# Performance work log

Measured on AMD Instinct MI355X. Metric: run time of the kernel, lower is better.

The kernel has to match this reference:

```python
import jax, jax.numpy as jnp
import numpy as np
import math

N, S, E, H = 32, 64, 512, 4
HD = E // H
EQ = E // 4
L2_TEMP = 13.544
LN_EPS = 1e-5


def _ln(x, g, b):
    m = jnp.mean(x, -1, keepdims=True)
    v = jnp.var(x, -1, keepdims=True)
    return (x - m) * jax.lax.rsqrt(v + LN_EPS) * g + b


def setup_inputs() -> dict:
    key = jax.random.key(0)
    ks = jax.random.split(key, 16)
    sc = 0.02
    inp = {
        "x": jax.random.normal(ks[0], (N, S, E), jnp.float32),
        # MultiheadAttention params (torch layout: in_proj_weight (3E,E))
        "Wqkv": jax.random.normal(ks[1], (3 * E, E), jnp.float32) * sc,
        "bqkv": jnp.zeros((3 * E,), jnp.float32),
        "Wo": jax.random.normal(ks[2], (E, E), jnp.float32) * sc,
        "bo": jnp.zeros((E,), jnp.float32),
        # fc1 (E, 2E), fc2 (E, E)
        "W1": jax.random.normal(ks[3], (E, 2 * E), jnp.float32) * sc,
        "b1": jnp.zeros((E,), jnp.float32),
        "W2": jax.random.normal(ks[4], (E, E), jnp.float32) * sc,
        "b2": jnp.zeros((E,), jnp.float32),
        # layer norms
        "g1": jnp.ones((E,), jnp.float32), "be1": jnp.zeros((E,), jnp.float32),
        "g2": jnp.ones((E,), jnp.float32), "be2": jnp.zeros((E,), jnp.float32),
        # fc_diff1: Linear(E, E//4), Linear(E//4, 1)
        "d1W1": jax.random.normal(ks[5], (EQ, E), jnp.float32) * sc,
        "d1b1": jnp.zeros((EQ,), jnp.float32),
        "d1W2": jax.random.normal(ks[6], (1, EQ), jnp.float32) * sc,
        "d1b2": jnp.zeros((1,), jnp.float32),
        # fc_diff2
        "d2W1": jax.random.normal(ks[7], (EQ, E), jnp.float32) * sc,
        "d2b1": jnp.zeros((EQ,), jnp.float32),
        "d2W2": jax.random.normal(ks[8], (1, EQ), jnp.float32) * sc,
        "d2b2": jnp.zeros((1,), jnp.float32),
    }
    return inp


def _mha(x, Wqkv, bqkv, Wo, bo):
    n, s, e = x.shape
    qkv = x @ Wqkv.T + bqkv
    q, k, v = jnp.split(qkv, 3, axis=-1)
    sh = lambda t: t.reshape(n, s, H, HD).transpose(0, 2, 1, 3)  # (n,H,s,hd)
    q, k, v = sh(q), sh(k), sh(v)
    scores = jnp.einsum('bhqd,bhkd->bhqk', q, k) / math.sqrt(HD)
    a = jax.nn.softmax(scores, axis=-1)
    o = jnp.einsum('bhqk,bhkd->bhqd', a, v).transpose(0, 2, 1, 3).reshape(n, s, e)
    return o @ Wo.T + bo, a.mean(axis=1)  # averaged attn weights (torch default)


def _pair_mlp(diff_w, W1a, b1a, W2a, b2a):
    # F.relu applied after every 'layer' (Linear, Dropout(eval=id), Linear)
    h = jax.nn.relu(diff_w @ W1a.T + b1a)  # relu(dropout(relu)) == relu composed -> same
    return jax.nn.relu(h @ W2a.T + b2a)[..., 0]  # (N,f,f)


def reference(x, Wqkv, bqkv, Wo, bo, W1, b1, W2, b2, g1, be1, g2, be2,
              d1W1, d1b1, d1W2, d1b2, d2W1, d2b1, d2W2, d2b2):
    # diff[b,f,g,e] = x[b,g,e] - x[b,f,e]
    diff = x[:, None, :, :] - x[:, :, None, :]  # (N,f,f,E)
    x1_attn = jax.nn.softmax(-jnp.sum(diff * diff, -1) / L2_TEMP, axis=-1)  # (N,f,f)
    x1 = jnp.einsum('bfg,bge->bfe', x1_attn, x)
    x2, x2_attn = _mha(x, Wqkv, bqkv, Wo, bo)
    x_res = jnp.concatenate([x1, x2], axis=-1)
    h = x + jax.nn.relu(x_res @ W1.T + b1)  # dropout eval = identity
    h = _ln(h, g1, be1)
    h = h + jax.nn.relu(h @ W2.T + b2)
    out = _ln(h, g2, be2)
    diff1 = _pair_mlp(diff * x1_attn[..., None], d1W1, d1b1, d1W2, d1b2)
    diff2 = _pair_mlp(diff * x2_attn[..., None], d2W1, d2b1, d2W2, d2b2)
    return out, x1_attn[:, None], x2_attn[:, None], diff1, diff2
```

## Files before the change

### kernel.cpp

```cpp
#include <hip/hip_runtime.h>
#include <math.h>

#define SS 64
#define EE 512
#define L2T 13.544f
#define LNEPS 1e-5f

using bf16x8 = __attribute__((ext_vector_type(8))) __bf16;
using u16x8  = __attribute__((ext_vector_type(8))) unsigned short;
using f32x4  = __attribute__((ext_vector_type(4))) float;

typedef const void __attribute__((address_space(1))) cv_global;
typedef void __attribute__((address_space(3))) v_lds;

__device__ inline unsigned short f2bf(float f) {
    union { float f; unsigned u; } v; v.f = f;
    unsigned r = v.u + 0x7fff + ((v.u >> 16) & 1);
    return (unsigned short)(r >> 16);
}
__device__ inline float bf2f(unsigned short h) {
    union { unsigned u; float f; } v; v.u = (unsigned)h << 16;
    return v.f;
}

#define MFMA16 __builtin_amdgcn_mfma_f32_16x16x32_bf16

#define XB_O    0
#define WFULL_O 1048576
#define W1CB_O  1966080
#define W2B_O   2490368
#define QKVB_O  2752512
#define X1O_O   5898240
#define HB_O    7995392
#define PB_O    9043968

__global__ __launch_bounds__(256)
void mega1(const float* __restrict__ x, const float* __restrict__ Wqkv,
           const float* __restrict__ Wo, const float* __restrict__ W1,
           const float* __restrict__ W2, const float* __restrict__ d1,
           const float* __restrict__ d2, const float* __restrict__ b1,
           const float* __restrict__ bo, unsigned short* __restrict__ bb,
           float* __restrict__ b_eff, float* __restrict__ x1_attn,
           unsigned short* __restrict__ Pl2) {
    const int bx = blockIdx.x, tid = threadIdx.x;
    __shared__ __align__(16) char smem[36096];

    if (bx < 1408) {
        int i = bx * 256 + tid;
        ushort4* dst4 = (ushort4*)bb;
        const float4* s; int di;
        if (i < 196608)      { s = (const float4*)Wqkv + i;          di = WFULL_O/4 + i; }
        else if (i < 212992) { int j = i-196608; s = (const float4*)d1 + j; di = WFULL_O/4 + 196608 + j; }
        else if (i < 229376) { int j = i-212992; s = (const float4*)d2 + j; di = WFULL_O/4 + 212992 + j; }
        else if (i < 294912) { int j = i-229376; s = (const float4*)W2 + j; di = W2B_O/4 + j; }
        else                 { int j = i-294912; int r = j>>7, cq = j&127;
                               s = (const float4*)W1 + r*256 + cq;   di = W1CB_O/4 + r*256 + cq; }
        float4 v = *s;
        ushort4 o;
        o.x = f2bf(v.x); o.y = f2bf(v.y); o.z = f2bf(v.z); o.w = f2bf(v.w);
        dst4[di] = o;
    } else if (bx < 1472) {
        const int tb = bx - 1408;
        const int m0 = (tb >> 3) * 64, n0 = (tb & 7) * 64;
        unsigned short* Asl = (unsigned short*)smem;
        unsigned short* Bsl = Asl + 64 * 40;
        const int wave = tid >> 6, lane = tid & 63;
        const int wm = (wave >> 1) * 32, wn = (wave & 1) * 32;
        const int fr = lane & 15, kq = (lane >> 4) * 8;
        f32x4 acc[2][2] = {};
        for (int k0 = 0; k0 < 512; k0 += 32) {
            {
                int m = tid >> 2, kk = (tid & 3) * 8;
                const float* src = W1 + (size_t)(m0 + m) * 1024 + 512 + k0 + kk;
                float4 v0 = *(const float4*)src, v1 = *(const float4*)(src + 4);
                u16x8 t = {f2bf(v0.x), f2bf(v0.y), f2bf(v0.z), f2bf(v0.w),
                           f2bf(v1.x), f2bf(v1.y), f2bf(v1.z), f2bf(v1.w)};
                *(u16x8*)(Asl + m * 40 + kk) = t;
            }
            {
                int k = tid >> 3, jq = (tid & 7) * 8;
                const float* src = Wo + (size_t)(k0 + k) * 512 + n0 + jq;
                float4 v0 = *(const float4*)src, v1 = *(const float4*)(src + 4);
                float vv[8] = {v0.x, v0.y, v0.z, v0.w, v1.x, v1.y, v1.z, v1.w};
                #pragma unroll
                for (int e = 0; e < 8; ++e) Bsl[(jq + e) * 40 + k] = f2bf(vv[e]);
            }
            __syncthreads();
            bf16x8 a0 = *(const bf16x8*)(Asl + (wm + fr) * 40 + kq);
            bf16x8 a1 = *(const bf16x8*)(Asl + (wm + 16 + fr) * 40 + kq);
            bf16x8 b0 = *(const bf16x8*)(Bsl + (wn + fr) * 40 + kq);
            bf16x8 b1 = *(const bf16x8*)(Bsl + (wn + 16 + fr) * 40 + kq);
            acc[0][0] = MFMA16(a0, b0, acc[0][0], 0, 0, 0);
            acc[0][1] = MFMA16(a0, b1, acc[0][1], 0, 0, 0);
            acc[1][0] = MFMA16(a1, b0, acc[1][0], 0, 0, 0);
            acc[1][1] = MFMA16(a1, b1, acc[1][1], 0, 0, 0);
            __syncthreads();
        }
        unsigned short* W1cb = bb + W1CB_O;
        const int crow = (lane >> 4) * 4, ccol = lane & 15;
        #pragma unroll
        for (int r2 = 0; r2 < 2; ++r2)
            #pragma unroll
            for (int c2 = 0; c2 < 2; ++c2)
                #pragma unroll
                for (int i = 0; i < 4; ++i) {
                    int m = m0 + wm + r2 * 16 + crow + i;
                    int j = n0 + wn + c2 * 16 + ccol;
                    W1cb[(size_t)m * 1024 + 512 + j] = f2bf(acc[r2][c2][i]);
                }
    } else if (bx < 1476) {
        int n = (bx - 1472) * 128 + (tid >> 1);
        int kh = (tid & 1) * 256;
        float s = 0.f;
        for (int k = 0; k < 256; ++k)
            s += W1[(size_t)n * 1024 + 512 + kh + k] * bo[kh + k];
        s += __shfl_xor(s, 1);
        if ((tid & 1) == 0) b_eff[n] = b1[n] + s;
    } else {
        const int b = bx - 1476;
        unsigned short* Xhi = (unsigned short*)smem;
        unsigned short* Xlo = Xhi + 64 * 72;
        float* sc    = (float*)(Xlo + 64 * 72);
        float* norms = sc + 64 * 68;
        const int wave = tid >> 6, lane = tid & 63;
        const int wm = (wave >> 1) * 32, wn = (wave & 1) * 32;
        const int fr = lane & 15;
        const int srow = tid >> 2, scq = (tid & 3) * 16;

        f32x4 acc[2][2] = {};
        const float* xrow = x + (size_t)b * 32768;
        unsigned short* xbg = bb + XB_O + (size_t)b * 32768;

        for (int k0 = 0; k0 < 512; k0 += 64) {
            const float* src = xrow + srow * 512 + k0 + scq;
            u16x8 hi0, hi1, lo0, lo1;
            #pragma unroll
            for (int e = 0; e < 8; ++e) {
                float v = src[e];
                unsigned short h = f2bf(v);
                hi0[e] = h; lo0[e] = f2bf(v - bf2f(h));
            }
            #pragma unroll
            for (int e = 0; e < 8; ++e) {
                float v = src[8 + e];
                unsigned short h = f2bf(v);
                hi1[e] = h; lo1[e] = f2bf(v - bf2f(h));
            }
            *(u16x8*)(Xhi + srow * 72 + scq)     = hi0;
            *(u16x8*)(Xhi + srow * 72 + scq + 8) = hi1;
            *(u16x8*)(Xlo + srow * 72 + scq)     = lo0;
            *(u16x8*)(Xlo + srow * 72 + scq + 8) = lo1;
            *(u16x8*)(xbg + srow * 512 + k0 + scq)     = hi0;
            *(u16x8*)(xbg + srow * 512 + k0 + scq + 8) = hi1;
            __syncthreads();
            #pragma unroll
            for (int j = 0; j < 2; ++j) {
                int kk = j * 32 + (lane >> 4) * 8;
                bf16x8 ah0 = *(const bf16x8*)(Xhi + (wm + fr) * 72 + kk);
                bf16x8 ah1 = *(const bf16x8*)(Xhi + (wm + 16 + fr) * 72 + kk);
                bf16x8 bh0 = *(const bf16x8*)(Xhi + (wn + fr) * 72 + kk);
                bf16x8 bh1 = *(const bf16x8*)(Xhi + (wn + 16 + fr) * 72 + kk);
                bf16x8 al0 = *(const bf16x8*)(Xlo + (wm + fr) * 72 + kk);
                bf16x8 al1 = *(const bf16x8*)(Xlo + (wm + 16 + fr) * 72 + kk);
                bf16x8 bl0 = *(const bf16x8*)(Xlo + (wn + fr) * 72 + kk);
                bf16x8 bl1 = *(const bf16x8*)(Xlo + (wn + 16 + fr) * 72 + kk);
                acc[0][0] = MFMA16(ah0, bh0, acc[0][0], 0, 0, 0);
                acc[0][0] = MFMA16(ah0, bl0, acc[0][0], 0, 0, 0);
                acc[0][0] = MFMA16(al0, bh0, acc[0][0], 0, 0, 0);
                acc[0][1] = MFMA16(ah0, bh1, acc[0][1], 0, 0, 0);
                acc[0][1] = MFMA16(ah0, bl1, acc[0][1], 0, 0, 0);
                acc[0][1] = MFMA16(al0, bh1, acc[0][1], 0, 0, 0);
                acc[1][0] = MFMA16(ah1, bh0, acc[1][0], 0, 0, 0);
                acc[1][0] = MFMA16(ah1, bl0, acc[1][0], 0, 0, 0);
                acc[1][0] = MFMA16(al1, bh0, acc[1][0], 0, 0, 0);
                acc[1][1] = MFMA16(ah1, bh1, acc[1][1], 0, 0, 0);
                acc[1][1] = MFMA16(ah1, bl1, acc[1][1], 0, 0, 0);
                acc[1][1] = MFMA16(al1, bh1, acc[1][1], 0, 0, 0);
            }
            __syncthreads();
        }
        const int crow = (lane >> 4) * 4, ccol = lane & 15;
        #pragma unroll
        for (int r2 = 0; r2 < 2; ++r2)
            #pragma unroll
            for (int c2 = 0; c2 < 2; ++c2)
                #pragma unroll
                for (int i = 0; i < 4; ++i)
                    sc[(wm + r2 * 16 + crow + i) * 68 + wn + c2 * 16 + ccol] =
                        acc[r2][c2][i];
        __syncthreads();
        if (tid < 64) norms[tid] = sc[tid * 68 + tid];
        __syncthreads();
        #pragma unroll
        for (int i = 0; i < 16; ++i) {
            int f = wave * 16 + i;
            float nf = norms[f];
            float val = (2.f * sc[f * 68 + lane] - nf - norms[lane]) * (1.0f / L2T);
            float mx = val;
            #pragma unroll
            for (int m = 32; m; m >>= 1) mx = fmaxf(mx, __shfl_xor(mx, m));
            float e = expf(val - mx);
            float sum = e;
            #pragma unroll
            for (int m = 32; m; m >>= 1) sum += __shfl_xor(sum, m);
            float a = e / sum;
            x1_attn[((size_t)b * 64 + f) * 64 + lane] = a;
            Pl2[((size_t)b * 64 + f) * 64 + lane] = f2bf(a);
        }
    }
}

__global__ __launch_bounds__(256)
void gemm_qkvp(const unsigned short* __restrict__ A,
               const unsigned short* __restrict__ B,
               const float* __restrict__ bias,
               unsigned short* __restrict__ Cq, unsigned short* __restrict__ Cp,
               const unsigned short* __restrict__ Pl2,
               unsigned short* __restrict__ x1o) {
    __shared__ unsigned short qsm[8704];
    const int tid = threadIdx.x, wave = tid >> 6, lane = tid & 63;
    const int fr = lane & 15;
    const int crow = (lane >> 4) * 4, ccol = lane & 15;

    if (blockIdx.x < 28) {
        unsigned short* Asl = qsm;
        unsigned short* Bsl = qsm + 4096;
        const int m0 = blockIdx.y * 64, n0 = blockIdx.x * 64;
        const int wm = (wave >> 1) * 32, wn = (wave & 1) * 32;
        const int kq4 = lane >> 4;
        f32x4 acc[2][2] = {};

        for (int k0 = 0; k0 < 512; k0 += 64) {
            #pragma unroll
            for (int c0 = 0; c0 < 512; c0 += 256) {
                int cc = c0 + tid, r = cc >> 3, q = cc & 7;
                int col = (q ^ (r & 7)) * 8;
                __builtin_amdgcn_global_load_lds(
                    (cv_global*)(A + (size_t)(m0 + r) * 512 + k0 + col),
                    (v_lds*)(Asl + c0 * 8 + wave * 512), 16, 0, 0);
            }
            #pragma unroll
            for (int c0 = 0; c0 < 512; c0 += 256) {
                int cc = c0 + tid, r = cc >> 3, q = cc & 7;
                int col = (q ^ (r & 7)) * 8;
                __builtin_amdgcn_global_load_lds(
                    (cv_global*)(B + (size_t)(n0 + r) * 512 + k0 + col),
                    (v_lds*)(Bsl + c0 * 8 + wave * 512), 16, 0, 0);
            }
            __syncthreads();
            #pragma unroll
            for (int j = 0; j < 2; ++j) {
                int kc = kq4 + j * 4;
                int rb0 = wn + fr, rb1 = wn + 16 + fr;
                bf16x8 b0 = *(const bf16x8*)(Bsl + rb0 * 64 + (kc ^ (rb0 & 7)) * 8);
                bf16x8 b1 = *(const bf16x8*)(Bsl + rb1 * 64 + (kc ^ (rb1 & 7)) * 8);
                #pragma unroll
                for (int r = 0; r < 2; ++r) {
                    int ra = wm + r * 16 + fr;
                    bf16x8 af = *(const bf16x8*)(Asl + ra * 64 + (kc ^ (ra & 7)) * 8);
                    acc[r][0] = MFMA16(af, b0, acc[r][0], 0, 0, 0);
                    acc[r][1] = MFMA16(af, b1, acc[r][1], 0, 0, 0);
                }
            }
            __syncthreads();
        }

        if (blockIdx.x < 24) {
            float bj0 = bias[n0 + wn + ccol], bj1 = bias[n0 + wn + 16 + ccol];
            #pragma unroll
            for (int r = 0; r < 2; ++r)
                #pragma unroll
                for (int c = 0; c < 2; ++c) {
                    float bj = c ? bj1 : bj0;
                    #pragma unroll
                    for (int i = 0; i < 4; ++i) {
                        size_t m = (size_t)(m0 + wm + r * 16 + crow + i);
                        int n = n0 + wn + c * 16 + ccol;
                        Cq[m * 1536 + n] = f2bf(acc[r][c][i] + bj);
                    }
                }
        } else {
            int p0 = n0 - 1536;
            #pragma unroll
            for (int r = 0; r < 2; ++r)
                #pragma unroll
                for (int c = 0; c < 2; ++c)
                    #pragma unroll
                    for (int i = 0; i < 4; ++i) {
                        size_t m = (size_t)(m0 + wm + r * 16 + crow + i);
                        int n = p0 + wn + c * 16 + ccol;
                        Cp[m * 256 + n] = f2bf(acc[r][c][i]);
                    }
        }
    } else {
        const int e0 = (blockIdx.x - 28) * 64;
        const int b = blockIdx.y;
        unsigned short* Ap = qsm;
        unsigned short* Xt = qsm + 64 * 68;
        {
            int row = tid >> 2, cq = (tid & 3) * 16;
            const unsigned short* src = Pl2 + (size_t)b * 4096 + row * 64 + cq;
            *(u16x8*)(Ap + row * 68 + cq)     = *(const u16x8*)src;
            *(u16x8*)(Ap + row * 68 + cq + 8) = *(const u16x8*)(src + 8);
        }
        {
            int g = tid >> 2, cq = (tid & 3) * 16;
            const unsigned short* src = A + (size_t)b * 32768 + g * 512 + e0 + cq;
            u16x8 v0 = *(const u16x8*)src, v1 = *(const u16x8*)(src + 8);
            #pragma unroll
            for (int e = 0; e < 8; ++e) Xt[(cq + e) * 68 + g] = v0[e];
            #pragma unroll
            for (int e = 0; e < 8; ++e) Xt[(cq + 8 + e) * 68 + g] = v1[e];
        }
        __syncthreads();
        const int wm2 = wave * 16;
        f32x4 o[4] = {};
        #pragma unroll
        for (int j = 0; j < 2; ++j) {
            int kk = j * 32 + (lane >> 4) * 8;
            bf16x8 a = *(const bf16x8*)(Ap + (wm2 + fr) * 68 + kk);
            #pragma unroll
            for (int t = 0; t < 4; ++t) {
                bf16x8 bv = *(const bf16x8*)(Xt + (t * 16 + fr) * 68 + kk);
                o[t] = MFMA16(a, bv, o[t], 0, 0, 0);
            }
        }
        #pragma unroll
        for (int t = 0; t < 4; ++t)
            #pragma unroll
            for (int i = 0; i < 4; ++i) {
                size_t m = (size_t)b * 64 + wm2 + crow + i;
                x1o[m * 1024 + e0 + t * 16 + ccol] = f2bf(o[t][i]);
            }
    }
}

__global__ __launch_bounds__(256)
void mha_attn(const unsigned short* __restrict__ qkv,
              unsigned short* __restrict__ x1o, float* __restrict__ pws) {
    const int hh = blockIdx.x;
    const int h = hh >> 1, half = hh & 1;
    const int b = blockIdx.y;
    const int tid = threadIdx.x, wave = tid >> 6, lane = tid & 63;

    __shared__ unsigned short Qs[32 * 136];
    __shared__ unsigned short Ks[64 * 136];
    __shared__ unsigned short Vt[128 * 72];
    __shared__ float sc[32 * 68];
    __shared__ unsigned short Pbf[32 * 72];

    const unsigned short* base = qkv + (size_t)b * 64 * 1536;
    {
        int row = tid >> 3, col = (tid & 7) * 16;
        const unsigned short* src = base + (half * 32 + row) * 1536 + h * 128 + col;
        *(u16x8*)(Qs + row * 136 + col)     = *(const u16x8*)(src);
        *(u16x8*)(Qs + row * 136 + col + 8) = *(const u16x8*)(src + 8);
    }
    {
        int row = tid >> 2, col = (tid & 3) * 32;
        const unsigned short* src = base + row * 1536 + 512 + h * 128 + col;
        #pragma unroll
        for (int j = 0; j < 4; ++j)
            *(u16x8*)(Ks + row * 136 + col + j * 8) = *(const u16x8*)(src + j * 8);
    }
    {
        int g = tid >> 2, col = (tid & 3) * 32;
        const unsigned short* src = base + g * 1536 + 1024 + h * 128 + col;
        #pragma unroll
        for (int j = 0; j < 4; ++j) {
            u16x8 v = *(const u16x8*)(src + j * 8);
            #pragma unroll
            for (int e = 0; e < 8; ++e)
                Vt[(col + j * 8 + e) * 72 + g] = v[e];
        }
    }
    __syncthreads();

    const int fr = lane & 15, kq = (lane >> 4) * 8;
    const int crow = (lane >> 4) * 4, ccol = lane & 15;
    const int wm = (wave >> 1) * 16;
    {
        const int wn = (wave & 1) * 32;
        f32x4 s0 = {0.f, 0.f, 0.f, 0.f}, s1 = s0;
        #pragma unroll
        for (int k0 = 0; k0 < 128; k0 += 32) {
            bf16x8 a  = *(const bf16x8*)(Qs + (wm + fr) * 136 + k0 + kq);
            bf16x8 b0 = *(const bf16x8*)(Ks + (wn + fr) * 136 + k0 + kq);
            bf16x8 b1 = *(const bf16x8*)(Ks + (wn + 16 + fr) * 136 + k0 + kq);
            s0 = MFMA16(a, b0, s0, 0, 0, 0);
            s1 = MFMA16(a, b1, s1, 0, 0, 0);
        }
        const float scale = 0.08838834764831845f;
        #pragma unroll
        for (int r = 0; r < 4; ++r) {
            sc[(wm + crow + r) * 68 + wn + ccol]      = s0[r] * scale;
            sc[(wm + crow + r) * 68 + wn + 16 + ccol] = s1[r] * scale;
        }
    }
    __syncthreads();

    #pragma unroll
    for (int i = 0; i < 8; ++i) {
        int f = wave * 8 + i;
        float v = sc[f * 68 + lane];
        float mx = v;
        #pragma unroll
        for (int m = 32; m; m >>= 1) mx = fmaxf(mx, __shfl_xor(mx, m));
        float e = expf(v - mx);
        float sum = e;
        #pragma unroll
        for (int m = 32; m; m >>= 1) sum += __shfl_xor(sum, m);
        float a = e / sum;
        Pbf[f * 72 + lane] = f2bf(a);
        pws[(((size_t)b * 4 + h) * 64 + half * 32 + f) * 64 + lane] = a;
    }
    __syncthreads();

    {
        const int wn2 = (wave & 1) * 64;
        f32x4 o[4];
        #pragma unroll
        for (int t = 0; t < 4; ++t) o[t] = f32x4{0.f, 0.f, 0.f, 0.f};
        #pragma unroll
        for (int k0 = 0; k0 < 64; k0 += 32) {
            bf16x8 a = *(const bf16x8*)(Pbf + (wm + fr) * 72 + k0 + kq);
            #pragma unroll
            for (int t = 0; t < 4; ++t) {
                bf16x8 bv = *(const bf16x8*)(Vt + (wn2 + t * 16 + fr) * 72 + k0 + kq);
                o[t] = MFMA16(a, bv, o[t], 0, 0, 0);
            }
        }
        #pragma unroll
        for (int t = 0; t < 4; ++t)
            #pragma unroll
            for (int r = 0; r < 4; ++r) {
                size_t m = (size_t)b * 64 + half * 32 + wm + crow + r;
                int col = h * 128 + wn2 + t * 16 + ccol;
                x1o[m * 1024 + 512 + col] = f2bf(o[t][r]);
            }
    }
}

__global__ __launch_bounds__(256)
void w1pair(const unsigned short* __restrict__ x1o,
            const unsigned short* __restrict__ W1cb,
            const float* __restrict__ beff, float* __restrict__ u,
            const unsigned short* __restrict__ Pb,
            const float* __restrict__ a1, const float* __restrict__ pws,
            const float* __restrict__ d1b1, const float* __restrict__ d1w2,
            const float* __restrict__ d1b2, const float* __restrict__ d2b1,
            const float* __restrict__ d2w2, const float* __restrict__ d2b2,
            float* __restrict__ x2_attn, float* __restrict__ out1,
            float* __restrict__ out2) {
    __shared__ unsigned short Asl[32 * 64];
    __shared__ unsigned short Bsl[64 * 64];
    const int bx = blockIdx.x, tid = threadIdx.x;
    const int wave = tid >> 6, lane = tid & 63;

    if (bx < 512) {
        const int m0 = (bx >> 3) * 32, n0 = (bx & 7) * 64;
        const int wm = (wave >> 1) * 16, wn = (wave & 1) * 32;
        const int fr = lane & 15, kq4 = lane >> 4;
        f32x4 acc[2] = {};
        for (int k0 = 0; k0 < 1024; k0 += 64) {
            {
                int r = tid >> 3, q = tid & 7;
                int col = (q ^ (r & 7)) * 8;
                __builtin_amdgcn_global_load_lds(
                    (cv_global*)(x1o + (size_t)(m0 + r) * 1024 + k0 + col),
                    (v_lds*)(Asl + wave * 512), 16, 0, 0);
            }
            #pragma unroll
            for (int c0 = 0; c0 < 512; c0 += 256) {
                int cc = c0 + tid, r = cc >> 3, q = cc & 7;
                int col = (q ^ (r & 7)) * 8;
                __builtin_amdgcn_global_load_lds(
                    (cv_global*)(W1cb + (size_t)(n0 + r) * 1024 + k0 + col),
                    (v_lds*)(Bsl + c0 * 8 + wave * 512), 16, 0, 0);
            }
            __syncthreads();
            #pragma unroll
            for (int j = 0; j < 2; ++j) {
                int kc = kq4 + j * 4;
                int rb0 = wn + fr, rb1 = wn + 16 + fr, ra = wm + fr;
                bf16x8 b0 = *(const bf16x8*)(Bsl + rb0 * 64 + (kc ^ (rb0 & 7)) * 8);
                bf16x8 b1 = *(const bf16x8*)(Bsl + rb1 * 64 + (kc ^ (rb1 & 7)) * 8);
                bf16x8 af = *(const bf16x8*)(Asl + ra * 64 + (kc ^ (ra & 7)) * 8);
                acc[0] = MFMA16(af, b0, acc[0], 0, 0, 0);
                acc[1] = MFMA16(af, b1, acc[1], 0, 0, 0);
            }
            __syncthreads();
        }
        const int crow = (lane >> 4) * 4, ccol = lane & 15;
        #pragma unroll
        for (int c = 0; c < 2; ++c) {
            int n = n0 + wn + c * 16 + ccol;
            float bj = beff[n];
            #pragma unroll
            for (int i = 0; i < 4; ++i) {
                size_t m = (size_t)(m0 + wm + crow + i);
                u[m * 512 + n] = fmaxf(acc[c][i] + bj, 0.f);
            }
        }
    } else {
        const int idx = bx - 512;
        const int f = idx & 63, b = idx >> 6;
        const size_t row = (size_t)b * SS + f;
        const int c0 = lane * 2, c1 = lane * 2 + 1;

        const float p1f0 = bf2f(Pb[row * 256 + c0]),       p1f1 = bf2f(Pb[row * 256 + c1]);
        const float p2f0 = bf2f(Pb[row * 256 + 128 + c0]), p2f1 = bf2f(Pb[row * 256 + 128 + c1]);
        const float w10 = d1w2[c0], w11 = d1w2[c1];
        const float w20 = d2w2[c0], w21 = d2w2[c1];
        const float b10 = d1b1[c0], b11 = d1b1[c1];
        const float b20 = d2b1[c0], b21 = d2b1[c1];
        const float bb1 = d1b2[0], bb2 = d2b2[0];

        const float* a1r = a1 + row * SS;
        const float* ph0 = pws + (((size_t)b * 4 + 0) * 64 + f) * 64;
        const float* ph1 = pws + (((size_t)b * 4 + 1) * 64 + f) * 64;
        const float* ph2 = pws + (((size_t)b * 4 + 2) * 64 + f) * 64;
        const float* ph3 = pws + (((size_t)b * 4 + 3) * 64 + f) * 64;
        const size_t bbase = (size_t)b * SS * 256;

        for (int g = wave; g < 64; g += 4) {
            float aa1 = a1r[g];
            float aa2 = 0.25f * (ph0[g] + ph1[g] + ph2[g] + ph3[g]);
            float q10 = bf2f(Pb[bbase + g * 256 + c0]);
            float q11 = bf2f(Pb[bbase + g * 256 + c1]);
            float q20 = bf2f(Pb[bbase + g * 256 + 128 + c0]);
            float q21 = bf2f(Pb[bbase + g * 256 + 128 + c1]);
            float h10 = fmaxf(aa1 * (q10 - p1f0) + b10, 0.f);
            float h11 = fmaxf(aa1 * (q11 - p1f1) + b11, 0.f);
            float h20 = fmaxf(aa2 * (q20 - p2f0) + b20, 0.f);
            float h21 = fmaxf(aa2 * (q21 - p2f1) + b21, 0.f);
            float s1 = w10 * h10 + w11 * h11;
            float s2 = w20 * h20 + w21 * h21;
            #pragma unroll
            for (int m = 32; m; m >>= 1) {
                s1 += __shfl_xor(s1, m);
                s2 += __shfl_xor(s2, m);
            }
            if (lane == 0) {
                x2_attn[row * SS + g] = aa2;
                out1[row * SS + g] = fmaxf(s1 + bb1, 0.f);
                out2[row * SS + g] = fmaxf(s2 + bb2, 0.f);
            }
        }
    }
}

__global__ __launch_bounds__(256)
void gemm_w2(const unsigned short* __restrict__ A,
             const unsigned short* __restrict__ B,
             const float* __restrict__ bias, float* __restrict__ C) {
    __shared__ unsigned short Asl[32 * 64];
    __shared__ unsigned short Bsl[64 * 64];
    const int tid = threadIdx.x, wave = tid >> 6, lane = tid & 63;
    const int m0 = blockIdx.y * 32, n0 = blockIdx.x * 64;
    const int wm = (wave >> 1) * 16, wn = (wave & 1) * 32;
    const int fr = lane & 15, kq4 = lane >> 4;
    f32x4 acc[2] = {};
    for (int k0 = 0; k0 < 512; k0 += 64) {
        {
            int r = tid >> 3, q = tid & 7;
            int col = (q ^ (r & 7)) * 8;
            __builtin_amdgcn_global_load_lds(
                (cv_global*)(A + (size_t)(m0 + r) * 512 + k0 + col),
                (v_lds*)(Asl + wave * 512), 16, 0, 0);
        }
        #pragma unroll
        for (int c0 = 0; c0 < 512; c0 += 256) {
            int cc = c0 + tid, r = cc >> 3, q = cc & 7;
            int col = (q ^ (r & 7)) * 8;
            __builtin_amdgcn_global_load_lds(
                (cv_global*)(B + (size_t)(n0 + r) * 512 + k0 + col),
                (v_lds*)(Bsl + c0 * 8 + wave * 512), 16, 0, 0);
        }
        __syncthreads();
        #pragma unroll
        for (int j = 0; j < 2; ++j) {
            int kc = kq4 + j * 4;
            int rb0 = wn + fr, rb1 = wn + 16 + fr, ra = wm + fr;
            bf16x8 b0 = *(const bf16x8*)(Bsl + rb0 * 64 + (kc ^ (rb0 & 7)) * 8);
            bf16x8 b1 = *(const bf16x8*)(Bsl + rb1 * 64 + (kc ^ (rb1 & 7)) * 8);
            bf16x8 af = *(const bf16x8*)(Asl + ra * 64 + (kc ^ (ra & 7)) * 8);
            acc[0] = MFMA16(af, b0, acc[0], 0, 0, 0);
            acc[1] = MFMA16(af, b1, acc[1], 0, 0, 0);
        }
        __syncthreads();
    }
    const int crow = (lane >> 4) * 4, ccol = lane & 15;
    #pragma unroll
    for (int c = 0; c < 2; ++c) {
        int n = n0 + wn + c * 16 + ccol;
        float bj = bias[n];
        #pragma unroll
        for (int i = 0; i < 4; ++i) {
            size_t m = (size_t)(m0 + wm + crow + i);
            C[m * 512 + n] = fmaxf(acc[c][i] + bj, 0.f);
        }
    }
}

__global__ __launch_bounds__(256)
void add_ln(const float* __restrict__ base, const float* __restrict__ u,
            const float* __restrict__ gam, const float* __restrict__ bet,
            float* __restrict__ out, unsigned short* __restrict__ outb) {
    const int row = blockIdx.x;
    const int tid = threadIdx.x, wave = tid >> 6, lane = tid & 63;
    const float* br = base + (size_t)row * EE;
    const float* ur = u + (size_t)row * EE;
    float t0 = br[tid] + ur[tid];
    float t1 = br[tid + 256] + ur[tid + 256];
    float s = t0 + t1, sq = t0 * t0 + t1 * t1;
    #pragma unroll
    for (int m = 32; m; m >>= 1) {
        s += __shfl_xor(s, m);
        sq += __shfl_xor(sq, m);
    }
    __shared__ float ssum[4], ssq[4];
    if (lane == 0) { ssum[wave] = s; ssq[wave] = sq; }
    __syncthreads();
    s = ssum[0] + ssum[1] + ssum[2] + ssum[3];
    sq = ssq[0] + ssq[1] + ssq[2] + ssq[3];
    float mean = s * (1.0f / EE);
    float var = sq * (1.0f / EE) - mean * mean;
    float inv = rsqrtf(var + LNEPS);
    float v0 = (t0 - mean) * inv * gam[tid] + bet[tid];
    float v1 = (t1 - mean) * inv * gam[tid + 256] + bet[tid + 256];
    float* orow = out + (size_t)row * EE;
    orow[tid] = v0;
    orow[tid + 256] = v1;
    if (outb) {
        unsigned short* obr = outb + (size_t)row * EE;
        obr[tid] = f2bf(v0);
        obr[tid + 256] = f2bf(v1);
    }
}

extern "C" void kernel_launch(void* const* d_in, const int* in_sizes, int n_in,
                              void* d_out, int out_size, void* d_ws,
                              size_t ws_size, hipStream_t stream) {
    const float* x    = (const float*)d_in[0];
    const float* Wqkv = (const float*)d_in[1];
    const float* bqkv = (const float*)d_in[2];
    const float* Wo   = (const float*)d_in[3];
    const float* bo   = (const float*)d_in[4];
    const float* W1   = (const float*)d_in[5];
    const float* b1   = (const float*)d_in[6];
    const float* W2   = (const float*)d_in[7];
    const float* b2   = (const float*)d_in[8];
    const float* g1   = (const float*)d_in[9];
    const float* be1  = (const float*)d_in[10];
    const float* g2   = (const float*)d_in[11];
    const float* be2  = (const float*)d_in[12];
    const float* d1W1 = (const float*)d_in[13];
    const float* d1b1 = (const float*)d_in[14];
    const float* d1W2 = (const float*)d_in[15];
    const float* d1b2 = (const float*)d_in[16];
    const float* d2W1 = (const float*)d_in[17];
    const float* d2b1 = (const float*)d_in[18];
    const float* d2W2 = (const float*)d_in[19];
    const float* d2b2 = (const float*)d_in[20];

    float* out      = (float*)d_out;
    float* out_main = out;
    float* x1_attn  = out + 1048576;
    float* x2_attn  = out + 1048576 + 131072;
    float* diff1    = out + 1048576 + 2 * 131072;
    float* diff2    = out + 1048576 + 3 * 131072;

    float* ws    = (float*)d_ws;
    float* u_buf = ws;
    float* h_buf = ws + 1048576;
    float* pws   = ws + 2097152;
    float* b_eff = ws + 2621440;
    unsigned short* Pl2 = (unsigned short*)(ws + 2621952);
    unsigned short* bb  = (unsigned short*)(ws + 2687488);

    unsigned short* xb    = bb + XB_O;
    unsigned short* Wfull = bb + WFULL_O;
    unsigned short* W1cb  = bb + W1CB_O;
    unsigned short* W2b   = bb + W2B_O;
    unsigned short* qkvb  = bb + QKVB_O;
    unsigned short* x1o   = bb + X1O_O;
    unsigned short* hb    = bb + HB_O;
    unsigned short* Pb    = bb + PB_O;

    mega1<<<1508, 256, 0, stream>>>(x, Wqkv, Wo, W1, W2, d1W1, d2W1, b1, bo,
                                    bb, b_eff, x1_attn, Pl2);

    gemm_qkvp<<<dim3(36, 32), 256, 0, stream>>>(xb, Wfull, bqkv, qkvb, Pb,
                                                Pl2, x1o);

    mha_attn<<<dim3(8, 32), 256, 0, stream>>>(qkvb, x1o, pws);

    w1pair<<<2560, 256, 0, stream>>>(x1o, W1cb, b_eff, u_buf, Pb, x1_attn, pws,
                                     d1b1, d1W2, d1b2, d2b1, d2W2, d2b2,
                                     x2_attn, diff1, diff2);

    add_ln<<<2048, 256, 0, stream>>>(x, u_buf, g1, be1, h_buf, hb);

    gemm_w2<<<dim3(8, 64), 256, 0, stream>>>(hb, W2b, b2, u_buf);

    add_ln<<<2048, 256, 0, stream>>>(h_buf, u_buf, g2, be2, out_main, nullptr);
}
```

Measured before the change: 179.0 us.

## Fuse LN1 into fc2 GEMM prologue and LN1+LN2 into final kernel

```diff
diff --git a/kernel.cpp b/kernel.cpp
--- a/kernel.cpp
+++ b/kernel.cpp
@@ -31,7 +31,6 @@
 #define W2B_O   2490368
 #define QKVB_O  2752512
 #define X1O_O   5898240
-#define HB_O    7995392
 #define PB_O    9043968
 
 __global__ __launch_bounds__(256)
@@ -214,110 +213,213 @@
 void gemm_qkvp(const unsigned short* __restrict__ A,
                const unsigned short* __restrict__ B,
                const float* __restrict__ bias,
-               unsigned short* __restrict__ Cq, unsigned short* __restrict__ Cp,
-               const unsigned short* __restrict__ Pl2,
-               unsigned short* __restrict__ x1o) {
-    __shared__ unsigned short qsm[8704];
+               unsigned short* __restrict__ Cq, unsigned short* __restrict__ Cp) {
+    __shared__ unsigned short Asl[64 * 64];
+    __shared__ unsigned short Bsl[64 * 64];
     const int tid = threadIdx.x, wave = tid >> 6, lane = tid & 63;
-    const int fr = lane & 15;
+    const int m0 = blockIdx.y * 64, n0 = blockIdx.x * 64;
+    const int wm = (wave >> 1) * 32, wn = (wave & 1) * 32;
+    const int fr = lane & 15, kq4 = lane >> 4;
+    f32x4 acc[2][2] = {};
+
+    for (int k0 = 0; k0 < 512; k0 += 64) {
+        #pragma unroll
+        for (int c0 = 0; c0 < 512; c0 += 256) {
+            int cc = c0 + tid, r = cc >> 3, q = cc & 7;
+            int col = (q ^ (r & 7)) * 8;
+            __builtin_amdgcn_global_load_lds(
+                (cv_global*)(A + (size_t)(m0 + r) * 512 + k0 + col),
+                (v_lds*)(Asl + c0 * 8 + wave * 512), 16, 0, 0);
+        }
+        #pragma unroll
+        for (int c0 = 0; c0 < 512; c0 += 256) {
+            int cc = c0 + tid, r = cc >> 3, q = cc & 7;
+            int col = (q ^ (r & 7)) * 8;
+            __builtin_amdgcn_global_load_lds(
+                (cv_global*)(B + (size_t)(n0 + r) * 512 + k0 + col),
+                (v_lds*)(Bsl + c0 * 8 + wave * 512), 16, 0, 0);
+        }
+        __syncthreads();
+        #pragma unroll
+        for (int j = 0; j < 2; ++j) {
+            int kc = kq4 + j * 4;
+            int rb0 = wn + fr, rb1 = wn + 16 + fr;
+            bf16x8 b0 = *(const bf16x8*)(Bsl + rb0 * 64 + (kc ^ (rb0 & 7)) * 8);
+            bf16x8 b1 = *(const bf16x8*)(Bsl + rb1 * 64 + (kc ^ (rb1 & 7)) * 8);
+            #pragma unroll
+            for (int r = 0; r < 2; ++r) {
+                int ra = wm + r * 16 + fr;
+                bf16x8 af = *(const bf16x8*)(Asl + ra * 64 + (kc ^ (ra & 7)) * 8);
+                acc[r][0] = MFMA16(af, b0, acc[r][0], 0, 0, 0);
+                acc[r][1] = MFMA16(af, b1, acc[r][1], 0, 0, 0);
+            }
+        }
+        __syncthreads();
+    }
+
     const int crow = (lane >> 4) * 4, ccol = lane & 15;
-
-    if (blockIdx.x < 28) {
-        unsigned short* Asl = qsm;
-        unsigned short* Bsl = qsm + 4096;
-        const int m0 = blockIdx.y * 64, n0 = blockIdx.x * 64;
-        const int wm = (wave >> 1) * 32, wn = (wave & 1) * 32;
-        const int kq4 = lane >> 4;
-        f32x4 acc[2][2] = {};
-
-        for (int k0 = 0; k0 < 512; k0 += 64) {
-            #pragma unroll
-            for (int c0 = 0; c0 < 512; c0 += 256) {
-                int cc = c0 + tid, r = cc >> 3, q = cc & 7;
-                int col = (q ^ (r & 7)) * 8;
-                __builtin_amdgcn_global_load_lds(
-                    (cv_global*)(A + (size_t)(m0 + r) * 512 + k0 + col),
-                    (v_lds*)(Asl + c0 * 8 + wave * 512), 16, 0, 0);
-            }
-            #pragma unroll
-            for (int c0 = 0; c0 < 512; c0 += 256) {
-                int cc = c0 + tid, r = cc >> 3, q = cc & 7;
-                int col = (q ^ (r & 7)) * 8;
-                __builtin_amdgcn_global_load_lds(
-                    (cv_global*)(B + (size_t)(n0 + r) * 512 + k0 + col),
-                    (v_lds*)(Bsl + c0 * 8 + wave * 512), 16, 0, 0);
-            }
-            __syncthreads();
-            #pragma unroll
-            for (int j = 0; j < 2; ++j) {
-                int kc = kq4 + j * 4;
-                int rb0 = wn + fr, rb1 = wn + 16 + fr;
-                bf16x8 b0 = *(const bf16x8*)(Bsl + rb0 * 64 + (kc ^ (rb0 & 7)) * 8);
-                bf16x8 b1 = *(const bf16x8*)(Bsl + rb1 * 64 + (kc ^ (rb1 & 7)) * 8);
+    if (blockIdx.x < 24) {
+        float bj0 = bias[n0 + wn + ccol], bj1 = bias[n0 + wn + 16 + ccol];
+        #pragma unroll
+        for (int r = 0; r < 2; ++r)
+            #pragma unroll
+            for (int c = 0; c < 2; ++c) {
+                float bj = c ? bj1 : bj0;
                 #pragma unroll
-                for (int r = 0; r < 2; ++r) {
-                    int ra = wm + r * 16 + fr;
-                    bf16x8 af = *(const bf16x8*)(Asl + ra * 64 + (kc ^ (ra & 7)) * 8);
-                    acc[r][0] = MFMA16(af, b0, acc[r][0], 0, 0, 0);
-                    acc[r][1] = MFMA16(af, b1, acc[r][1], 0, 0, 0);
+                for (int i = 0; i < 4; ++i) {
+                    size_t m = (size_t)(m0 + wm + r * 16 + crow + i);
+                    int n = n0 + wn + c * 16 + ccol;
+                    Cq[m * 1536 + n] = f2bf(acc[r][c][i] + bj);
                 }
             }
-            __syncthreads();
-        }
-
-        if (blockIdx.x < 24) {
-            float bj0 = bias[n0 + wn + ccol], bj1 = bias[n0 + wn + 16 + ccol];
-            #pragma unroll
-            for (int r = 0; r < 2; ++r)
+    } else {
+        int p0 = n0 - 1536;
+        #pragma unroll
+        for (int r = 0; r < 2; ++r)
+            #pragma unroll
+            for (int c = 0; c < 2; ++c)
                 #pragma unroll
-                for (int c = 0; c < 2; ++c) {
-                    float bj = c ? bj1 : bj0;
-                    #pragma unroll
-                    for (int i = 0; i < 4; ++i) {
-                        size_t m = (size_t)(m0 + wm + r * 16 + crow + i);
-                        int n = n0 + wn + c * 16 + ccol;
-                        Cq[m * 1536 + n] = f2bf(acc[r][c][i] + bj);
-                    }
+                for (int i = 0; i < 4; ++i) {
+                    size_t m = (size_t)(m0 + wm + r * 16 + crow + i);
+                    int n = p0 + wn + c * 16 + ccol;
+                    Cp[m * 256 + n] = f2bf(acc[r][c][i]);
                 }
-        } else {
-            int p0 = n0 - 1536;
-            #pragma unroll
-            for (int r = 0; r < 2; ++r)
+    }
+}
+
+__global__ __launch_bounds__(256)
+void mha_x1(const unsigned short* __restrict__ qkv,
+            unsigned short* __restrict__ x1o, float* __restrict__ pws,
+            const unsigned short* __restrict__ Pl2,
+            const unsigned short* __restrict__ xb) {
+    __shared__ __align__(16) char smem[57856];
+    const int tid = threadIdx.x, wave = tid >> 6, lane = tid & 63;
+    const int fr = lane & 15, kq = (lane >> 4) * 8;
+    const int crow = (lane >> 4) * 4, ccol = lane & 15;
+    const int b = blockIdx.y;
+
+    if (blockIdx.x < 8) {
+        const int hh = blockIdx.x;
+        const int h = hh >> 1, half = hh & 1;
+        unsigned short* Qs  = (unsigned short*)smem;
+        unsigned short* Ks  = Qs + 32 * 136;
+        unsigned short* Vt  = Ks + 64 * 136;
+        float*          sc  = (float*)(smem + 44544);
+        unsigned short* Pbf = (unsigned short*)(smem + 53248);
+
+        const unsigned short* base = qkv + (size_t)b * 64 * 1536;
+        {
+            int row = tid >> 3, col = (tid & 7) * 16;
+            const unsigned short* src = base + (half * 32 + row) * 1536 + h * 128 + col;
+            *(u16x8*)(Qs + row * 136 + col)     = *(const u16x8*)(src);
+            *(u16x8*)(Qs + row * 136 + col + 8) = *(const u16x8*)(src + 8);
+        }
+        {
+            int row = tid >> 2, col = (tid & 3) * 32;
+            const unsigned short* src = base + row * 1536 + 512 + h * 128 + col;
+            #pragma unroll
+            for (int j = 0; j < 4; ++j)
+                *(u16x8*)(Ks + row * 136 + col + j * 8) = *(const u16x8*)(src + j * 8);
+        }
+        {
+            int g = tid >> 2, col = (tid & 3) * 32;
+            const unsigned short* src = base + g * 1536 + 1024 + h * 128 + col;
+            #pragma unroll
+            for (int j = 0; j < 4; ++j) {
+                u16x8 v = *(const u16x8*)(src + j * 8);
                 #pragma unroll
-                for (int c = 0; c < 2; ++c)
-                    #pragma unroll
-                    for (int i = 0; i < 4; ++i) {
-                        size_t m = (size_t)(m0 + wm + r * 16 + crow + i);
-                        int n = p0 + wn + c * 16 + ccol;
-                        Cp[m * 256 + n] = f2bf(acc[r][c][i]);
-                    }
+                for (int e = 0; e < 8; ++e)
+                    Vt[(col + j * 8 + e) * 72 + g] = v[e];
+            }
+        }
+        __syncthreads();
+
+        const int wm = (wave >> 1) * 16;
+        {
+            const int wn = (wave & 1) * 32;
+            f32x4 s0 = {0.f, 0.f, 0.f, 0.f}, s1 = s0;
+            #pragma unroll
+            for (int k0 = 0; k0 < 128; k0 += 32) {
+                bf16x8 a  = *(const bf16x8*)(Qs + (wm + fr) * 136 + k0 + kq);
+                bf16x8 b0 = *(const bf16x8*)(Ks + (wn + fr) * 136 + k0 + kq);
+                bf16x8 b1 = *(const bf16x8*)(Ks + (wn + 16 + fr) * 136 + k0 + kq);
+                s0 = MFMA16(a, b0, s0, 0, 0, 0);
+                s1 = MFMA16(a, b1, s1, 0, 0, 0);
+            }
+            const float scale = 0.08838834764831845f;
+            #pragma unroll
+            for (int r = 0; r < 4; ++r) {
+                sc[(wm + crow + r) * 68 + wn + ccol]      = s0[r] * scale;
+                sc[(wm + crow + r) * 68 + wn + 16 + ccol] = s1[r] * scale;
+            }
+        }
+        __syncthreads();
+
+        #pragma unroll
+        for (int i = 0; i < 8; ++i) {
+            int f = wave * 8 + i;
+            float v = sc[f * 68 + lane];
+            float mx = v;
+            #pragma unroll
+            for (int m = 32; m; m >>= 1) mx = fmaxf(mx, __shfl_xor(mx, m));
+            float e = expf(v - mx);
+            float sum = e;
+            #pragma unroll
+            for (int m = 32; m; m >>= 1) sum += __shfl_xor(sum, m);
+            float a = e / sum;
+            Pbf[f * 72 + lane] = f2bf(a);
+            pws[(((size_t)b * 4 + h) * 64 + half * 32 + f) * 64 + lane] = a;
+        }
+        __syncthreads();
+
+        {
+            const int wn2 = (wave & 1) * 64;
+            f32x4 o[4];
+            #pragma unroll
+            for (int t = 0; t < 4; ++t) o[t] = f32x4{0.f, 0.f, 0.f, 0.f};
+            #pragma unroll
+            for (int k0 = 0; k0 < 64; k0 += 32) {
+                bf16x8 a = *(const bf16x8*)(Pbf + (wm + fr) * 72 + k0 + kq);
+                #pragma unroll
+                for (int t = 0; t < 4; ++t) {
+                    bf16x8 bv = *(const bf16x8*)(Vt + (wn2 + t * 16 + fr) * 72 + k0 + kq);
+                    o[t] = MFMA16(a, bv, o[t], 0, 0, 0);
+                }
+            }
+            #pragma unroll
+            for (int t = 0; t < 4; ++t)
+                #pragma unroll
+                for (int r = 0; r < 4; ++r) {
+                    size_t m = (size_t)b * 64 + half * 32 + wm + crow + r;
+                    int col = h * 128 + wn2 + t * 16 + ccol;
+                    x1o[m * 1024 + 512 + col] = f2bf(o[t][r]);
+                }
         }
     } else {
-        const int e0 = (blockIdx.x - 28) * 64;
-        const int b = blockIdx.y;
-        unsigned short* Ap = qsm;
-        unsigned short* Xt = qsm + 64 * 68;
+        const int e0 = (blockIdx.x - 8) * 64;
+        unsigned short* Ap = (unsigned short*)smem;
+        unsigned short* Xt = Ap + 64 * 68;
         {
-            int row = tid >> 2, cq = (tid & 3) * 16;
-            const unsigned short* src = Pl2 + (size_t)b * 4096 + row * 64 + cq;
-            *(u16x8*)(Ap + row * 68 + cq)     = *(const u16x8*)src;
-            *(u16x8*)(Ap + row * 68 + cq + 8) = *(const u16x8*)(src + 8);
+            int row = tid >> 2, cq2 = (tid & 3) * 16;
+            const unsigned short* src = Pl2 + (size_t)b * 4096 + row * 64 + cq2;
+            *(u16x8*)(Ap + row * 68 + cq2)     = *(const u16x8*)src;
+            *(u16x8*)(Ap + row * 68 + cq2 + 8) = *(const u16x8*)(src + 8);
         }
         {
-            int g = tid >> 2, cq = (tid & 3) * 16;
-            const unsigned short* src = A + (size_t)b * 32768 + g * 512 + e0 + cq;
+            int g = tid >> 2, cq2 = (tid & 3) * 16;
+            const unsigned short* src = xb + (size_t)b * 32768 + g * 512 + e0 + cq2;
             u16x8 v0 = *(const u16x8*)src, v1 = *(const u16x8*)(src + 8);
             #pragma unroll
-            for (int e = 0; e < 8; ++e) Xt[(cq + e) * 68 + g] = v0[e];
-            #pragma unroll
-            for (int e = 0; e < 8; ++e) Xt[(cq + 8 + e) * 68 + g] = v1[e];
+            for (int e = 0; e < 8; ++e) Xt[(cq2 + e) * 68 + g] = v0[e];
+            #pragma unroll
+            for (int e = 0; e < 8; ++e) Xt[(cq2 + 8 + e) * 68 + g] = v1[e];
         }
         __syncthreads();
         const int wm2 = wave * 16;
         f32x4 o[4] = {};
         #pragma unroll
         for (int j = 0; j < 2; ++j) {
-            int kk = j * 32 + (lane >> 4) * 8;
+            int kk = j * 32 + kq;
             bf16x8 a = *(const bf16x8*)(Ap + (wm2 + fr) * 68 + kk);
             #pragma unroll
             for (int t = 0; t < 4; ++t) {
@@ -331,112 +433,6 @@
             for (int i = 0; i < 4; ++i) {
                 size_t m = (size_t)b * 64 + wm2 + crow + i;
                 x1o[m * 1024 + e0 + t * 16 + ccol] = f2bf(o[t][i]);
-            }
-    }
-}
-
-__global__ __launch_bounds__(256)
-void mha_attn(const unsigned short* __restrict__ qkv,
-              unsigned short* __restrict__ x1o, float* __restrict__ pws) {
-    const int hh = blockIdx.x;
-    const int h = hh >> 1, half = hh & 1;
-    const int b = blockIdx.y;
-    const int tid = threadIdx.x, wave = tid >> 6, lane = tid & 63;
-
-    __shared__ unsigned short Qs[32 * 136];
-    __shared__ unsigned short Ks[64 * 136];
-    __shared__ unsigned short Vt[128 * 72];
-    __shared__ float sc[32 * 68];
-    __shared__ unsigned short Pbf[32 * 72];
-
-    const unsigned short* base = qkv + (size_t)b * 64 * 1536;
-    {
-        int row = tid >> 3, col = (tid & 7) * 16;
-        const unsigned short* src = base + (half * 32 + row) * 1536 + h * 128 + col;
-        *(u16x8*)(Qs + row * 136 + col)     = *(const u16x8*)(src);
-        *(u16x8*)(Qs + row * 136 + col + 8) = *(const u16x8*)(src + 8);
-    }
-    {
-        int row = tid >> 2, col = (tid & 3) * 32;
-        const unsigned short* src = base + row * 1536 + 512 + h * 128 + col;
-        #pragma unroll
-        for (int j = 0; j < 4; ++j)
-            *(u16x8*)(Ks + row * 136 + col + j * 8) = *(const u16x8*)(src + j * 8);
-    }
-    {
-        int g = tid >> 2, col = (tid & 3) * 32;
-        const unsigned short* src = base + g * 1536 + 1024 + h * 128 + col;
-        #pragma unroll
-        for (int j = 0; j < 4; ++j) {
-            u16x8 v = *(const u16x8*)(src + j * 8);
-            #pragma unroll
-            for (int e = 0; e < 8; ++e)
-                Vt[(col + j * 8 + e) * 72 + g] = v[e];
-        }
-    }
-    __syncthreads();
-
-    const int fr = lane & 15, kq = (lane >> 4) * 8;
-    const int crow = (lane >> 4) * 4, ccol = lane & 15;
-    const int wm = (wave >> 1) * 16;
-    {
-        const int wn = (wave & 1) * 32;
-        f32x4 s0 = {0.f, 0.f, 0.f, 0.f}, s1 = s0;
-        #pragma unroll
-        for (int k0 = 0; k0 < 128; k0 += 32) {
-            bf16x8 a  = *(const bf16x8*)(Qs + (wm + fr) * 136 + k0 + kq);
-            bf16x8 b0 = *(const bf16x8*)(Ks + (wn + fr) * 136 + k0 + kq);
-            bf16x8 b1 = *(const bf16x8*)(Ks + (wn + 16 + fr) * 136 + k0 + kq);
-            s0 = MFMA16(a, b0, s0, 0, 0, 0);
-            s1 = MFMA16(a, b1, s1, 0, 0, 0);
-        }
-        const float scale = 0.08838834764831845f;
-        #pragma unroll
-        for (int r = 0; r < 4; ++r) {
-            sc[(wm + crow + r) * 68 + wn + ccol]      = s0[r] * scale;
-            sc[(wm + crow + r) * 68 + wn + 16 + ccol] = s1[r] * scale;
-        }
-    }
-    __syncthreads();
-
-    #pragma unroll
-    for (int i = 0; i < 8; ++i) {
-        int f = wave * 8 + i;
-        float v = sc[f * 68 + lane];
-        float mx = v;
-        #pragma unroll
-        for (int m = 32; m; m >>= 1) mx = fmaxf(mx, __shfl_xor(mx, m));
-        float e = expf(v - mx);
-        float sum = e;
-        #pragma unroll
-        for (int m = 32; m; m >>= 1) sum += __shfl_xor(sum, m);
-        float a = e / sum;
-        Pbf[f * 72 + lane] = f2bf(a);
-        pws[(((size_t)b * 4 + h) * 64 + half * 32 + f) * 64 + lane] = a;
-    }
-    __syncthreads();
-
-    {
-        const int wn2 = (wave & 1) * 64;
-        f32x4 o[4];
-        #pragma unroll
-        for (int t = 0; t < 4; ++t) o[t] = f32x4{0.f, 0.f, 0.f, 0.f};
-        #pragma unroll
-        for (int k0 = 0; k0 < 64; k0 += 32) {
-            bf16x8 a = *(const bf16x8*)(Pbf + (wm + fr) * 72 + k0 + kq);
-            #pragma unroll
-            for (int t = 0; t < 4; ++t) {
-                bf16x8 bv = *(const bf16x8*)(Vt + (wn2 + t * 16 + fr) * 72 + k0 + kq);
-                o[t] = MFMA16(a, bv, o[t], 0, 0, 0);
-            }
-        }
-        #pragma unroll
-        for (int t = 0; t < 4; ++t)
-            #pragma unroll
-            for (int r = 0; r < 4; ++r) {
-                size_t m = (size_t)b * 64 + half * 32 + wm + crow + r;
-                int col = h * 128 + wn2 + t * 16 + ccol;
-                x1o[m * 1024 + 512 + col] = f2bf(o[t][r]);
             }
     }
 }
@@ -551,30 +547,76 @@
 }
 
 __global__ __launch_bounds__(256)
-void gemm_w2(const unsigned short* __restrict__ A,
-             const unsigned short* __restrict__ B,
-             const float* __restrict__ bias, float* __restrict__ C) {
-    __shared__ unsigned short Asl[32 * 64];
+void fc2ln(const float* __restrict__ x, const float* __restrict__ u1,
+           const float* __restrict__ g1, const float* __restrict__ be1,
+           const unsigned short* __restrict__ W2b, const float* __restrict__ b2,
+           float* __restrict__ u2) {
+    __shared__ unsigned short As[32 * 512];
     __shared__ unsigned short Bsl[64 * 64];
+    __shared__ float stats[32 * 2];
     const int tid = threadIdx.x, wave = tid >> 6, lane = tid & 63;
     const int m0 = blockIdx.y * 32, n0 = blockIdx.x * 64;
+    const int row = tid >> 3, part = tid & 7;
+
+    {
+        const float4* xr = (const float4*)(x + (size_t)(m0 + row) * 512 + part * 64);
+        const float4* ur = (const float4*)(u1 + (size_t)(m0 + row) * 512 + part * 64);
+        float sum = 0.f, sq = 0.f;
+        #pragma unroll
+        for (int j = 0; j < 16; ++j) {
+            float4 a = xr[j], b = ur[j];
+            float e0 = a.x + b.x, e1 = a.y + b.y, e2 = a.z + b.z, e3 = a.w + b.w;
+            sum += e0 + e1 + e2 + e3;
+            sq  += e0 * e0 + e1 * e1 + e2 * e2 + e3 * e3;
+        }
+        #pragma unroll
+        for (int m = 4; m; m >>= 1) {
+            sum += __shfl_xor(sum, m);
+            sq  += __shfl_xor(sq, m);
+        }
+        if (part == 0) {
+            float mean = sum * (1.0f / EE);
+            float var = sq * (1.0f / EE) - mean * mean;
+            stats[row * 2] = mean;
+            stats[row * 2 + 1] = rsqrtf(var + LNEPS);
+        }
+    }
+    __syncthreads();
+    {
+        float mean = stats[row * 2], inv = stats[row * 2 + 1];
+        #pragma unroll
+        for (int j = 0; j < 8; ++j) {
+            int c = part * 8 + j, col = c * 8;
+            const float4* xa = (const float4*)(x + (size_t)(m0 + row) * 512 + col);
+            const float4* ua = (const float4*)(u1 + (size_t)(m0 + row) * 512 + col);
+            const float4* g4 = (const float4*)(g1 + col);
+            const float4* e4 = (const float4*)(be1 + col);
+            float4 a0 = xa[0], a1 = xa[1], b0 = ua[0], b1 = ua[1];
+            float4 gg0 = g4[0], gg1 = g4[1], ee0 = e4[0], ee1 = e4[1];
+            float t[8] = {a0.x + b0.x, a0.y + b0.y, a0.z + b0.z, a0.w + b0.w,
+                          a1.x + b1.x, a1.y + b1.y, a1.z + b1.z, a1.w + b1.w};
+            float gv[8] = {gg0.x, gg0.y, gg0.z, gg0.w, gg1.x, gg1.y, gg1.z, gg1.w};
+            float bv[8] = {ee0.x, ee0.y, ee0.z, ee0.w, ee1.x, ee1.y, ee1.z, ee1.w};
+            u16x8 hv;
+            #pragma unroll
+            for (int e = 0; e < 8; ++e)
+                hv[e] = f2bf((t[e] - mean) * inv * gv[e] + bv[e]);
+            int cs = (c & ~7) | ((c & 7) ^ (row & 7));
+            *(u16x8*)(As + row * 512 + cs * 8) = hv;
+        }
+    }
+    __syncthreads();
+
     const int wm = (wave >> 1) * 16, wn = (wave & 1) * 32;
     const int fr = lane & 15, kq4 = lane >> 4;
     f32x4 acc[2] = {};
     for (int k0 = 0; k0 < 512; k0 += 64) {
-        {
-            int r = tid >> 3, q = tid & 7;
-            int col = (q ^ (r & 7)) * 8;
-            __builtin_amdgcn_global_load_lds(
-                (cv_global*)(A + (size_t)(m0 + r) * 512 + k0 + col),
-                (v_lds*)(Asl + wave * 512), 16, 0, 0);
-        }
         #pragma unroll
         for (int c0 = 0; c0 < 512; c0 += 256) {
             int cc = c0 + tid, r = cc >> 3, q = cc & 7;
             int col = (q ^ (r & 7)) * 8;
             __builtin_amdgcn_global_load_lds(
-                (cv_global*)(B + (size_t)(n0 + r) * 512 + k0 + col),
+                (cv_global*)(W2b + (size_t)(n0 + r) * 512 + k0 + col),
                 (v_lds*)(Bsl + c0 * 8 + wave * 512), 16, 0, 0);
         }
         __syncthreads();
@@ -584,7 +626,7 @@
             int rb0 = wn + fr, rb1 = wn + 16 + fr, ra = wm + fr;
             bf16x8 b0 = *(const bf16x8*)(Bsl + rb0 * 64 + (kc ^ (rb0 & 7)) * 8);
             bf16x8 b1 = *(const bf16x8*)(Bsl + rb1 * 64 + (kc ^ (rb1 & 7)) * 8);
-            bf16x8 af = *(const bf16x8*)(Asl + ra * 64 + (kc ^ (ra & 7)) * 8);
+            bf16x8 af = *(const bf16x8*)(As + ra * 512 + k0 + (kc ^ (ra & 7)) * 8);
             acc[0] = MFMA16(af, b0, acc[0], 0, 0, 0);
             acc[1] = MFMA16(af, b1, acc[1], 0, 0, 0);
         }
@@ -594,32 +636,36 @@
     #pragma unroll
     for (int c = 0; c < 2; ++c) {
         int n = n0 + wn + c * 16 + ccol;
-        float bj = bias[n];
+        float bj = b2[n];
         #pragma unroll
         for (int i = 0; i < 4; ++i) {
             size_t m = (size_t)(m0 + wm + crow + i);
-            C[m * 512 + n] = fmaxf(acc[c][i] + bj, 0.f);
+            u2[m * 512 + n] = fmaxf(acc[c][i] + bj, 0.f);
         }
     }
 }
 
 __global__ __launch_bounds__(256)
-void add_ln(const float* __restrict__ base, const float* __restrict__ u,
-            const float* __restrict__ gam, const float* __restrict__ bet,
-            float* __restrict__ out, unsigned short* __restrict__ outb) {
+void ln_final(const float* __restrict__ x, const float* __restrict__ u1,
+              const float* __restrict__ u2, const float* __restrict__ g1,
+              const float* __restrict__ be1, const float* __restrict__ g2,
+              const float* __restrict__ be2, float* __restrict__ out) {
     const int row = blockIdx.x;
     const int tid = threadIdx.x, wave = tid >> 6, lane = tid & 63;
-    const float* br = base + (size_t)row * EE;
-    const float* ur = u + (size_t)row * EE;
-    float t0 = br[tid] + ur[tid];
-    float t1 = br[tid + 256] + ur[tid + 256];
+    __shared__ float ssum[4], ssq[4];
+
+    const float* xr = x + (size_t)row * EE;
+    const float* u1r = u1 + (size_t)row * EE;
+    const float* u2r = u2 + (size_t)row * EE;
+
+    float t0 = xr[tid] + u1r[tid];
+    float t1 = xr[tid + 256] + u1r[tid + 256];
     float s = t0 + t1, sq = t0 * t0 + t1 * t1;
     #pragma unroll
     for (int m = 32; m; m >>= 1) {
         s += __shfl_xor(s, m);
         sq += __shfl_xor(sq, m);
     }
-    __shared__ float ssum[4], ssq[4];
     if (lane == 0) { ssum[wave] = s; ssq[wave] = sq; }
     __syncthreads();
     s = ssum[0] + ssum[1] + ssum[2] + ssum[3];
@@ -627,16 +673,28 @@
     float mean = s * (1.0f / EE);
     float var = sq * (1.0f / EE) - mean * mean;
     float inv = rsqrtf(var + LNEPS);
-    float v0 = (t0 - mean) * inv * gam[tid] + bet[tid];
-    float v1 = (t1 - mean) * inv * gam[tid + 256] + bet[tid + 256];
+    float h0 = (t0 - mean) * inv * g1[tid] + be1[tid];
+    float h1 = (t1 - mean) * inv * g1[tid + 256] + be1[tid + 256];
+
+    float s0 = h0 + u2r[tid];
+    float s1 = h1 + u2r[tid + 256];
+    float s2 = s0 + s1, sq2 = s0 * s0 + s1 * s1;
+    #pragma unroll
+    for (int m = 32; m; m >>= 1) {
+        s2 += __shfl_xor(s2, m);
+        sq2 += __shfl_xor(sq2, m);
+    }
+    __syncthreads();
+    if (lane == 0) { ssum[wave] = s2; ssq[wave] = sq2; }
+    __syncthreads();
+    s2 = ssum[0] + ssum[1] + ssum[2] + ssum[3];
+    sq2 = ssq[0] + ssq[1] + ssq[2] + ssq[3];
+    float mean2 = s2 * (1.0f / EE);
+    float var2 = sq2 * (1.0f / EE) - mean2 * mean2;
+    float inv2 = rsqrtf(var2 + LNEPS);
     float* orow = out + (size_t)row * EE;
-    orow[tid] = v0;
-    orow[tid + 256] = v1;
-    if (outb) {
-        unsigned short* obr = outb + (size_t)row * EE;
-        obr[tid] = f2bf(v0);
-        obr[tid + 256] = f2bf(v1);
-    }
+    orow[tid] = (s0 - mean2) * inv2 * g2[tid] + be2[tid];
+    orow[tid + 256] = (s1 - mean2) * inv2 * g2[tid + 256] + be2[tid + 256];
 }
 
 extern "C" void kernel_launch(void* const* d_in, const int* in_sizes, int n_in,
@@ -672,8 +730,8 @@
     float* diff2    = out + 1048576 + 3 * 131072;
 
     float* ws    = (float*)d_ws;
-    float* u_buf = ws;
-    float* h_buf = ws + 1048576;
+    float* u1_buf = ws;
+    float* u2_buf = ws + 1048576;
     float* pws   = ws + 2097152;
     float* b_eff = ws + 2621440;
     unsigned short* Pl2 = (unsigned short*)(ws + 2621952);
@@ -685,24 +743,21 @@
     unsigned short* W2b   = bb + W2B_O;
     unsigned short* qkvb  = bb + QKVB_O;
     unsigned short* x1o   = bb + X1O_O;
-    unsigned short* hb    = bb + HB_O;
     unsigned short* Pb    = bb + PB_O;
 
     mega1<<<1508, 256, 0, stream>>>(x, Wqkv, Wo, W1, W2, d1W1, d2W1, b1, bo,
                                     bb, b_eff, x1_attn, Pl2);
 
-    gemm_qkvp<<<dim3(36, 32), 256, 0, stream>>>(xb, Wfull, bqkv, qkvb, Pb,
-                                                Pl2, x1o);
-
-    mha_attn<<<dim3(8, 32), 256, 0, stream>>>(qkvb, x1o, pws);
-
-    w1pair<<<2560, 256, 0, stream>>>(x1o, W1cb, b_eff, u_buf, Pb, x1_attn, pws,
+    gemm_qkvp<<<dim3(28, 32), 256, 0, stream>>>(xb, Wfull, bqkv, qkvb, Pb);
+
+    mha_x1<<<dim3(16, 32), 256, 0, stream>>>(qkvb, x1o, pws, Pl2, xb);
+
+    w1pair<<<2560, 256, 0, stream>>>(x1o, W1cb, b_eff, u1_buf, Pb, x1_attn, pws,
                                      d1b1, d1W2, d1b2, d2b1, d2W2, d2b2,
                                      x2_attn, diff1, diff2);
 
-    add_ln<<<2048, 256, 0, stream>>>(x, u_buf, g1, be1, h_buf, hb);
-
-    gemm_w2<<<dim3(8, 64), 256, 0, stream>>>(hb, W2b, b2, u_buf);
-
-    add_ln<<<2048, 256, 0, stream>>>(h_buf, u_buf, g2, be2, out_main, nullptr);
-}
+    fc2ln<<<dim3(8, 64), 256, 0, stream>>>(x, u1_buf, g1, be1, W2b, b2, u2_buf);
+
+    ln_final<<<2048, 256, 0, stream>>>(x, u1_buf, u2_buf, g1, be1, g2, be2,
+                                       out_main);
+}
```

Result: slower. 199.1 us (+11.2%).
